# Optimization experiments

Measured on AMD Instinct MI355X. Metric: run time of the kernel, lower is better.

The kernel has to match this reference:

```python
import jax, jax.numpy as jnp
import numpy as np

DIM = 768
NUM_HEADS = 12
HEAD_DIM = DIM // NUM_HEADS
B, N = 8, 1024


def setup_inputs() -> dict:
    key = jax.random.key(0)
    ks = jax.random.split(key, 6)
    s = 0.02
    return {
        "x": jax.random.normal(ks[0], (B, N, DIM), dtype=jnp.float32),
        "context": jax.random.normal(ks[1], (B, N, DIM), dtype=jnp.float32),
        "qkv_w": jax.random.normal(ks[2], (DIM, 3 * DIM), dtype=jnp.float32) * s,
        "qkv_b": jnp.zeros((3 * DIM,), dtype=jnp.float32),
        "proj_w": jax.random.normal(ks[3], (DIM, DIM), dtype=jnp.float32) * s,
        "proj_b": jnp.zeros((DIM,), dtype=jnp.float32),
    }


def reference(x, context, qkv_w, qkv_b, proj_w, proj_b):
    # NOTE: original layer ignores `context` (computes q,k,v all from x).
    b, n, c = x.shape
    h, d = NUM_HEADS, c // NUM_HEADS
    scale = d ** -0.5
    qkv = x @ qkv_w + qkv_b                      # [B, N, 3C]
    qkv = qkv.reshape(b, n, 3, h, d)
    qkv = jnp.transpose(qkv, (2, 0, 3, 1, 4))    # [3, B, H, N, d]
    q, k, v = qkv[0], qkv[1], qkv[2]
    attn = jnp.einsum("bhqd,bhkd->bhqk", q * scale, k)  # [B, H, N, N]
    attn = jax.nn.softmax(attn, axis=-1)
    out = jnp.einsum("bhqk,bhkd->bhqd", attn, v)         # [B, H, N, d]
    out = jnp.transpose(out, (0, 2, 1, 3)).reshape(b, n, c)
    return out @ proj_w + proj_b
```

## Files before the change

### kernel.cpp

```cpp
#include <hip/hip_runtime.h>
#include <hip/hip_bf16.h>
#include <math.h>

#define DIM 768
#define NH 12
#define HD 64
#define BB 8
#define NN 1024
#define M_TOK (BB*NN)

#define QSCALE 0.18033688011112042f

typedef __bf16 bf16x8 __attribute__((ext_vector_type(8)));
typedef float  f32x4  __attribute__((ext_vector_type(4)));
typedef float  f32x16 __attribute__((ext_vector_type(16)));

__device__ __forceinline__ ushort f2bf(float f) {
  unsigned u = __float_as_uint(f);
  u += 0x7FFF + ((u >> 16) & 1);
  return (ushort)(u >> 16);
}

__global__ void k_prep(const float* __restrict__ x, ushort* __restrict__ x_bf,
                       const float* __restrict__ qkv_w, ushort* __restrict__ qkv_wT,
                       const float* __restrict__ proj_w, ushort* __restrict__ proj_wT) {
  __shared__ ushort tile[64 * 65];
  int bid = blockIdx.x;
  int t = threadIdx.x;
  if (bid < 6144) {
    int i = bid * 256 + t;
    float4 v = ((const float4*)x)[i];
    ushort4 o; o.x = f2bf(v.x); o.y = f2bf(v.y); o.z = f2bf(v.z); o.w = f2bf(v.w);
    ((ushort4*)x_bf)[i] = o;
    return;
  }
  const float* w; ushort* wt; int N;
  int tb = bid - 6144;
  if (tb < 432) { w = qkv_w; wt = qkv_wT; N = 3 * DIM; }
  else          { tb -= 432; w = proj_w; wt = proj_wT; N = DIM; }
  int nbx = N >> 6;
  int n0 = (tb % nbx) * 64, k0 = (tb / nbx) * 64;
  for (int i = 0; i < 16; i++) {
    int flat = i * 256 + t;
    int r = flat >> 6, c = flat & 63;
    tile[c * 65 + r] = f2bf(w[(size_t)(k0 + r) * N + n0 + c]);
  }
  __syncthreads();
  for (int i = 0; i < 16; i++) {
    int flat = i * 256 + t;
    int r = flat >> 6, c = flat & 63;
    wt[(size_t)(n0 + r) * DIM + k0 + c] = tile[r * 65 + c];
  }
}

__device__ __forceinline__ bf16x8 lds_ld(const ushort* base, int row, int col8) {
  return *(const bf16x8*)((const char*)base + (((row << 3) + (col8 ^ (row & 7))) << 4));
}

#define GLL(g, l) __builtin_amdgcn_global_load_lds((const __attribute__((address_space(1))) void*)(g), (__attribute__((address_space(3))) void*)(l), 16, 0, 0)

template<int EPI, int BM>
__global__ __launch_bounds__(256) void k_gemm(
    const ushort* __restrict__ A, const ushort* __restrict__ Bt,
    const float* __restrict__ bias, int M, int N, int K,
    float* __restrict__ outF,
    ushort* __restrict__ qo, ushort* __restrict__ ko, ushort* __restrict__ vo)
{
  __shared__ ushort a_lds[BM * 64];
  __shared__ ushort b_lds[128 * 64];
  constexpr int NR = (BM == 128) ? 4 : 2;
  int tid = threadIdx.x;
  int wave = tid >> 6, lane = tid & 63;
  int lr = lane & 15, lg = lane >> 4;
  int rowb = (BM == 128) ? (wave >> 1) * 64 : 0;
  int colb = (BM == 128) ? (wave & 1) * 64 : wave * 32;
  int nbx = N >> 7;
  int nwg = nbx * (M / BM);
  int id = blockIdx.x;
  int nid = (id & 7) * (nwg >> 3) + (id >> 3);
  int bcol = (nid % nbx) << 7;
  int brow = (nid / nbx) * BM;

  f32x4 acc[4][NR] = {};
  for (int k0 = 0; k0 < K; k0 += 64) {
    __syncthreads();
    #pragma unroll
    for (int i = 0; i < BM / 32; i++) {
      int l = i * 256 + tid;
      int row = l >> 3;
      int cg = (l & 7) ^ (row & 7);
      GLL(A + (size_t)(brow + row) * K + k0 + cg * 8, (char*)a_lds + i * 4096 + wave * 1024);
    }
    #pragma unroll
    for (int i = 0; i < 4; i++) {
      int l = i * 256 + tid;
      int row = l >> 3;
      int cg = (l & 7) ^ (row & 7);
      GLL(Bt + (size_t)(bcol + row) * K + k0 + cg * 8, (char*)b_lds + i * 4096 + wave * 1024);
    }
    __syncthreads();
    #pragma unroll
    for (int ks = 0; ks < 2; ks++) {
      bf16x8 af[4], bfr[NR];
      #pragma unroll
      for (int mi = 0; mi < 4; mi++)
        af[mi] = lds_ld(a_lds, rowb + mi * 16 + lr, ks * 4 + lg);
      #pragma unroll
      for (int ni = 0; ni < NR; ni++)
        bfr[ni] = lds_ld(b_lds, colb + ni * 16 + lr, ks * 4 + lg);
      #pragma unroll
      for (int mi = 0; mi < 4; mi++)
        #pragma unroll
        for (int ni = 0; ni < NR; ni++)
          acc[mi][ni] = __builtin_amdgcn_mfma_f32_16x16x32_bf16(af[mi], bfr[ni], acc[mi][ni], 0, 0, 0);
    }
  }
  #pragma unroll
  for (int mi = 0; mi < 4; mi++)
    #pragma unroll
    for (int ni = 0; ni < NR; ni++) {
      if constexpr (EPI == 0) {
        int gm0 = brow + rowb + mi * 16 + lg * 4;
        int gc = bcol + colb + ni * 16 + lr;
        float bs = bias[gc];
        int which = (gc >= 1536) ? 2 : (gc >= 768 ? 1 : 0);
        int f = gc - which * 768;
        int h = f >> 6, dd = f & 63;
        int b = gm0 >> 10, np = gm0 & 1023;
        int bh = b * NH + h;
        if (which == 2) {
          ushort4 pk;
          pk.x = f2bf(acc[mi][ni][0] + bs);
          pk.y = f2bf(acc[mi][ni][1] + bs);
          pk.z = f2bf(acc[mi][ni][2] + bs);
          pk.w = f2bf(acc[mi][ni][3] + bs);
          *(ushort4*)&vo[((size_t)bh * HD + dd) * NN + np] = pk;
        } else if (which == 0) {
          #pragma unroll
          for (int i = 0; i < 4; i++)
            qo[((size_t)bh * NN + np + i) * HD + dd] = f2bf((acc[mi][ni][i] + bs) * QSCALE);
        } else {
          #pragma unroll
          for (int i = 0; i < 4; i++)
            ko[((size_t)bh * NN + np + i) * HD + dd] = f2bf(acc[mi][ni][i] + bs);
        }
      } else {
        #pragma unroll
        for (int i = 0; i < 4; i++) {
          int gm = brow + rowb + mi * 16 + lg * 4 + i;
          int gc = bcol + colb + ni * 16 + lr;
          outF[(size_t)gm * N + gc] = acc[mi][ni][i] + bias[gc];
        }
      }
    }
}

__global__ __launch_bounds__(256) void k_attn(
    const ushort* __restrict__ Q, const ushort* __restrict__ Kk,
    const ushort* __restrict__ Vt, ushort* __restrict__ Oo)
{
  __shared__ ushort k_lds[2][64 * 64];
  __shared__ ushort v_lds[2][64 * 64];
  int tid = threadIdx.x;
  int wave = tid >> 6, lane = tid & 63;
  int lq = lane & 31;
  int hh = lane >> 5;
  int hid = blockIdx.x;
  int xcd = hid & 7;
  int rr = hid >> 3;
  int qb = rr / 12;
  int bhi = rr % 12;
  int bh = bhi * 8 + xcd;
  int q0 = qb * 128;
  int b = bh / NH, h = bh % NH;

  int l0 = tid, l1 = 256 + tid;
  int row0 = l0 >> 3, cg0 = (l0 & 7) ^ (row0 & 7);
  int row1 = l1 >> 3, cg1 = (l1 & 7) ^ (row1 & 7);
  const char* kp0 = (const char*)(Kk + ((size_t)bh * NN + row0) * HD + cg0 * 8);
  const char* kp1 = (const char*)(Kk + ((size_t)bh * NN + row1) * HD + cg1 * 8);
  const char* vp0 = (const char*)(Vt + ((size_t)bh * HD + row0) * NN + cg0 * 8);
  const char* vp1 = (const char*)(Vt + ((size_t)bh * HD + row1) * NN + cg1 * 8);

  auto stage = [&](int kt, int buf) {
    size_t ko = (size_t)kt * (64 * HD * 2);
    size_t vo = (size_t)kt * (64 * 2);
    GLL(kp0 + ko, (char*)&k_lds[buf][0] + wave * 1024);
    GLL(kp1 + ko, (char*)&k_lds[buf][0] + 4096 + wave * 1024);
    GLL(vp0 + vo, (char*)&v_lds[buf][0] + wave * 1024);
    GLL(vp1 + vo, (char*)&v_lds[buf][0] + 4096 + wave * 1024);
  };

  int qrow = q0 + wave * 32 + lq;
  bf16x8 qf[4];
  #pragma unroll
  for (int dks = 0; dks < 4; dks++)
    qf[dks] = *(const bf16x8*)&Q[((size_t)bh * NN + qrow) * HD + dks * 16 + hh * 8];

  f32x16 o0 = {}, o1 = {};
  float l_run = 0.f;

  stage(0, 0);
  __syncthreads();

  for (int kt = 0; kt < 16; kt++) {
    int cur = kt & 1;
    if (kt < 15) stage(kt + 1, cur ^ 1);
    f32x16 s0 = {}, s1 = {};
    #pragma unroll
    for (int dks = 0; dks < 4; dks++) {
      bf16x8 kf0 = lds_ld(&k_lds[cur][0], lq,      dks * 2 + hh);
      bf16x8 kf1 = lds_ld(&k_lds[cur][0], 32 + lq, dks * 2 + hh);
      s0 = __builtin_amdgcn_mfma_f32_32x32x16_bf16(kf0, qf[dks], s0, 0, 0, 0);
      s1 = __builtin_amdgcn_mfma_f32_32x32x16_bf16(kf1, qf[dks], s1, 0, 0, 0);
    }
    #pragma unroll
    for (int j = 0; j < 16; j++) { s0[j] = __builtin_amdgcn_exp2f(s0[j]); l_run += s0[j]; }
    #pragma unroll
    for (int j = 0; j < 16; j++) { s1[j] = __builtin_amdgcn_exp2f(s1[j]); l_run += s1[j]; }
    auto pv = [&](const f32x16& P, int kt2) {
      #pragma unroll
      for (int kb = 0; kb < 2; kb++) {
        int ks = kt2 * 2 + kb;
        int r0 = kb * 8;
        int a0, a1, c0, c1;
        asm("v_cvt_pk_bf16_f32 %0, %1, %2" : "=v"(a0) : "v"(P[r0 + 0]), "v"(P[r0 + 1]));
        asm("v_cvt_pk_bf16_f32 %0, %1, %2" : "=v"(a1) : "v"(P[r0 + 2]), "v"(P[r0 + 3]));
        asm("v_cvt_pk_bf16_f32 %0, %1, %2" : "=v"(c0) : "v"(P[r0 + 4]), "v"(P[r0 + 5]));
        asm("v_cvt_pk_bf16_f32 %0, %1, %2" : "=v"(c1) : "v"(P[r0 + 6]), "v"(P[r0 + 7]));
        asm("v_permlane32_swap_b32 %0, %1" : "+v"(a0), "+v"(c0));
        asm("v_permlane32_swap_b32 %0, %1" : "+v"(a1), "+v"(c1));
        int4 w; w.x = a0; w.y = a1; w.z = c0; w.w = c1;
        bf16x8 pb = *(bf16x8*)&w;
        bf16x8 vf0 = lds_ld(&v_lds[cur][0], lq,      ks * 2 + hh);
        bf16x8 vf1 = lds_ld(&v_lds[cur][0], 32 + lq, ks * 2 + hh);
        o0 = __builtin_amdgcn_mfma_f32_32x32x16_bf16(vf0, pb, o0, 0, 0, 0);
        o1 = __builtin_amdgcn_mfma_f32_32x32x16_bf16(vf1, pb, o1, 0, 0, 0);
      }
    };
    pv(s0, 0);
    pv(s1, 1);
    if (kt < 15) __syncthreads();
  }
  l_run += __shfl_xor(l_run, 32);
  float inv = 1.0f / l_run;
  #pragma unroll
  for (int dt = 0; dt < 2; dt++) {
    const f32x16& o = dt ? o1 : o0;
    #pragma unroll
    for (int g = 0; g < 4; g++) {
      ushort4 pk;
      pk.x = f2bf(o[g * 4 + 0] * inv);
      pk.y = f2bf(o[g * 4 + 1] * inv);
      pk.z = f2bf(o[g * 4 + 2] * inv);
      pk.w = f2bf(o[g * 4 + 3] * inv);
      *(ushort4*)&Oo[((size_t)b * NN + qrow) * DIM + h * HD + dt * 32 + g * 8 + hh * 4] = pk;
    }
  }
}

extern "C" void kernel_launch(void* const* d_in, const int* in_sizes, int n_in,
                              void* d_out, int out_size, void* d_ws, size_t ws_size,
                              hipStream_t stream) {
  const float* x      = (const float*)d_in[0];
  const float* qkv_w  = (const float*)d_in[2];
  const float* qkv_b  = (const float*)d_in[3];
  const float* proj_w = (const float*)d_in[4];
  const float* proj_b = (const float*)d_in[5];
  float* out = (float*)d_out;

  char* ws = (char*)d_ws;
  size_t off = 0;
  auto alloc = [&](size_t bytes) { char* p = ws + off; off += (bytes + 255) & ~255ull; return p; };
  ushort* x_bf    = (ushort*)alloc((size_t)M_TOK * DIM * 2);
  ushort* qkv_wT  = (ushort*)alloc((size_t)DIM * 3 * DIM * 2);
  ushort* proj_wT = (ushort*)alloc((size_t)DIM * DIM * 2);
  ushort* q_arr   = (ushort*)alloc((size_t)M_TOK * DIM * 2);
  ushort* k_arr   = (ushort*)alloc((size_t)M_TOK * DIM * 2);
  ushort* vt_arr  = (ushort*)alloc((size_t)M_TOK * DIM * 2);
  ushort* attn_out = x_bf;

  k_prep<<<6720, 256, 0, stream>>>(x, x_bf, qkv_w, qkv_wT, proj_w, proj_wT);
  k_gemm<0, 128><<<(3 * DIM / 128) * (M_TOK / 128), 256, 0, stream>>>(
      x_bf, qkv_wT, qkv_b, M_TOK, 3 * DIM, DIM, nullptr, q_arr, k_arr, vt_arr);
  k_attn<<<BB * NH * (NN / 128), 256, 0, stream>>>(q_arr, k_arr, vt_arr, attn_out);
  k_gemm<1, 64><<<(DIM / 128) * (M_TOK / 64), 256, 0, stream>>>(
      attn_out, proj_wT, proj_b, M_TOK, DIM, DIM, out, nullptr, nullptr, nullptr);
}
```

Measured before the change: 106.9 us.

## Load K/V fragments directly from global memory, dropping LDS staging and barriers

The attention kernel no longer stages K and V tiles through double-buffered shared memory with async global-to-LDS loads and per-tile barriers. Each wave now loads its MFMA operand fragments straight from global memory into registers, and launch bounds ask for three blocks per CU. This removes LDS traffic and synchronisation, but the four waves of a block now each fetch the same K/V data separately, relying on L1/L2 to absorb the repeats. There is also no software prefetch, so global load latency is exposed unless occupancy hides it.

```diff
diff --git a/kernel.cpp b/kernel.cpp
--- a/kernel.cpp
+++ b/kernel.cpp
@@ -155,12 +155,10 @@
     }
 }
 
-__global__ __launch_bounds__(256) void k_attn(
+__global__ __launch_bounds__(256, 3) void k_attn(
     const ushort* __restrict__ Q, const ushort* __restrict__ Kk,
     const ushort* __restrict__ Vt, ushort* __restrict__ Oo)
 {
-  __shared__ ushort k_lds[2][64 * 64];
-  __shared__ ushort v_lds[2][64 * 64];
   int tid = threadIdx.x;
   int wave = tid >> 6, lane = tid & 63;
   int lq = lane & 31;
@@ -174,45 +172,38 @@
   int q0 = qb * 128;
   int b = bh / NH, h = bh % NH;
 
-  int l0 = tid, l1 = 256 + tid;
-  int row0 = l0 >> 3, cg0 = (l0 & 7) ^ (row0 & 7);
-  int row1 = l1 >> 3, cg1 = (l1 & 7) ^ (row1 & 7);
-  const char* kp0 = (const char*)(Kk + ((size_t)bh * NN + row0) * HD + cg0 * 8);
-  const char* kp1 = (const char*)(Kk + ((size_t)bh * NN + row1) * HD + cg1 * 8);
-  const char* vp0 = (const char*)(Vt + ((size_t)bh * HD + row0) * NN + cg0 * 8);
-  const char* vp1 = (const char*)(Vt + ((size_t)bh * HD + row1) * NN + cg1 * 8);
-
-  auto stage = [&](int kt, int buf) {
-    size_t ko = (size_t)kt * (64 * HD * 2);
-    size_t vo = (size_t)kt * (64 * 2);
-    GLL(kp0 + ko, (char*)&k_lds[buf][0] + wave * 1024);
-    GLL(kp1 + ko, (char*)&k_lds[buf][0] + 4096 + wave * 1024);
-    GLL(vp0 + vo, (char*)&v_lds[buf][0] + wave * 1024);
-    GLL(vp1 + vo, (char*)&v_lds[buf][0] + 4096 + wave * 1024);
-  };
-
   int qrow = q0 + wave * 32 + lq;
   bf16x8 qf[4];
   #pragma unroll
   for (int dks = 0; dks < 4; dks++)
     qf[dks] = *(const bf16x8*)&Q[((size_t)bh * NN + qrow) * HD + dks * 16 + hh * 8];
 
+  const ushort* kp0 = Kk + ((size_t)bh * NN + lq) * HD + hh * 8;
+  const ushort* kp1 = kp0 + 32 * HD;
+  const ushort* vp0 = Vt + ((size_t)bh * HD + lq) * NN + hh * 8;
+  const ushort* vp1 = vp0 + 32 * NN;
+
   f32x16 o0 = {}, o1 = {};
   float l_run = 0.f;
 
-  stage(0, 0);
-  __syncthreads();
-
   for (int kt = 0; kt < 16; kt++) {
-    int cur = kt & 1;
-    if (kt < 15) stage(kt + 1, cur ^ 1);
+    bf16x8 kl[4], kh[4];
+    #pragma unroll
+    for (int d = 0; d < 4; d++) {
+      kl[d] = *(const bf16x8*)(kp0 + (size_t)kt * 64 * HD + d * 16);
+      kh[d] = *(const bf16x8*)(kp1 + (size_t)kt * 64 * HD + d * 16);
+    }
+    bf16x8 vl[4], vh[4];
+    #pragma unroll
+    for (int s = 0; s < 4; s++) {
+      vl[s] = *(const bf16x8*)(vp0 + kt * 64 + s * 16);
+      vh[s] = *(const bf16x8*)(vp1 + kt * 64 + s * 16);
+    }
     f32x16 s0 = {}, s1 = {};
     #pragma unroll
     for (int dks = 0; dks < 4; dks++) {
-      bf16x8 kf0 = lds_ld(&k_lds[cur][0], lq,      dks * 2 + hh);
-      bf16x8 kf1 = lds_ld(&k_lds[cur][0], 32 + lq, dks * 2 + hh);
-      s0 = __builtin_amdgcn_mfma_f32_32x32x16_bf16(kf0, qf[dks], s0, 0, 0, 0);
-      s1 = __builtin_amdgcn_mfma_f32_32x32x16_bf16(kf1, qf[dks], s1, 0, 0, 0);
+      s0 = __builtin_amdgcn_mfma_f32_32x32x16_bf16(kl[dks], qf[dks], s0, 0, 0, 0);
+      s1 = __builtin_amdgcn_mfma_f32_32x32x16_bf16(kh[dks], qf[dks], s1, 0, 0, 0);
     }
     #pragma unroll
     for (int j = 0; j < 16; j++) { s0[j] = __builtin_amdgcn_exp2f(s0[j]); l_run += s0[j]; }
@@ -232,15 +223,12 @@
         asm("v_permlane32_swap_b32 %0, %1" : "+v"(a1), "+v"(c1));
         int4 w; w.x = a0; w.y = a1; w.z = c0; w.w = c1;
         bf16x8 pb = *(bf16x8*)&w;
-        bf16x8 vf0 = lds_ld(&v_lds[cur][0], lq,      ks * 2 + hh);
-        bf16x8 vf1 = lds_ld(&v_lds[cur][0], 32 + lq, ks * 2 + hh);
-        o0 = __builtin_amdgcn_mfma_f32_32x32x16_bf16(vf0, pb, o0, 0, 0, 0);
-        o1 = __builtin_amdgcn_mfma_f32_32x32x16_bf16(vf1, pb, o1, 0, 0, 0);
+        o0 = __builtin_amdgcn_mfma_f32_32x32x16_bf16(vl[ks], pb, o0, 0, 0, 0);
+        o1 = __builtin_amdgcn_mfma_f32_32x32x16_bf16(vh[ks], pb, o1, 0, 0, 0);
       }
     };
     pv(s0, 0);
     pv(s1, 1);
-    if (kt < 15) __syncthreads();
   }
   l_run += __shfl_xor(l_run, 32);
   float inv = 1.0f / l_run;
```

Result: slower. 160.5 us (+50.2%).
